# Optimization experiments

Measured on AMD Instinct MI355X. Metric: run time of the kernel, lower is better.

Reference implementation:

```python
import jax, jax.numpy as jnp
import numpy as np

D = 256
H = 8
FFN = 2048
EPS = 1e-5


def _layer_norm(x, g, b):
    m = jnp.mean(x, axis=-1, keepdims=True)
    v = jnp.mean((x - m) ** 2, axis=-1, keepdims=True)
    return (x - m) * jax.lax.rsqrt(v + EPS) * g + b


def _mha(q_in, k_in, v_in, wq, bq, wk, bk, wv, bv, wo, bo, mask):
    B, Sq, _ = q_in.shape
    Sk = k_in.shape[1]
    dh = D // H
    q = (q_in @ wq + bq).reshape(B, Sq, H, dh)
    k = (k_in @ wk + bk).reshape(B, Sk, H, dh)
    v = (v_in @ wv + bv).reshape(B, Sk, H, dh)
    scores = jnp.einsum('bqhd,bkhd->bhqk', q, k) / jnp.sqrt(jnp.float32(dh)).astype(q.dtype)
    if mask is not None:
        scores = scores + mask
    probs = jax.nn.softmax(scores, axis=-1)
    ctx = jnp.einsum('bhqk,bkhd->bqhd', probs, v).reshape(B, Sq, D)
    return ctx @ wo + bo


def setup_inputs() -> dict:
    key = jax.random.key(0)
    ks = jax.random.split(key, 32)
    s = 0.02
    def lin(i, din, dout):
        return jax.random.normal(ks[i], (din, dout), jnp.float32) * s
    inp = {
        'vision_encoder_hidden_states': jax.random.normal(ks[0], (4, 2048, D), jnp.float32),
        'text_encoder_hidden_states': jax.random.normal(ks[1], (4, 1024, D), jnp.float32),
        'vision_encoder_attention_mask': jnp.zeros((4, 1, 1, 2048), jnp.float32),
        'text_encoder_attention_mask': jnp.zeros((4, 1, 1, 1024), jnp.float32),
        'sa_wq': lin(2, D, D), 'sa_bq': jnp.zeros((D,), jnp.float32),
        'sa_wk': lin(3, D, D), 'sa_bk': jnp.zeros((D,), jnp.float32),
        'sa_wv': lin(4, D, D), 'sa_bv': jnp.zeros((D,), jnp.float32),
        'sa_wo': lin(5, D, D), 'sa_bo': jnp.zeros((D,), jnp.float32),
        'ca_wq': lin(6, D, D), 'ca_bq': jnp.zeros((D,), jnp.float32),
        'ca_wk': lin(7, D, D), 'ca_bk': jnp.zeros((D,), jnp.float32),
        'ca_wv': lin(8, D, D), 'ca_bv': jnp.zeros((D,), jnp.float32),
        'ca_wo': lin(9, D, D), 'ca_bo': jnp.zeros((D,), jnp.float32),
        'ln1_g': jnp.ones((D,), jnp.float32), 'ln1_b': jnp.zeros((D,), jnp.float32),
        'ln2_g': jnp.ones((D,), jnp.float32), 'ln2_b': jnp.zeros((D,), jnp.float32),
        'ln3_g': jnp.ones((D,), jnp.float32), 'ln3_b': jnp.zeros((D,), jnp.float32),
        'ln4_g': jnp.ones((D,), jnp.float32), 'ln4_b': jnp.zeros((D,), jnp.float32),
        'fc1_w': lin(10, D, FFN), 'fc1_b': jnp.zeros((FFN,), jnp.float32),
        'fc2_w': lin(11, FFN, D), 'fc2_b': jnp.zeros((D,), jnp.float32),
    }
    return inp


def reference(vision_encoder_hidden_states, text_encoder_hidden_states,
              vision_encoder_attention_mask, text_encoder_attention_mask,
              sa_wq, sa_bq, sa_wk, sa_bk, sa_wv, sa_bv, sa_wo, sa_bo,
              ca_wq, ca_bq, ca_wk, ca_bk, ca_wv, ca_bv, ca_wo, ca_bo,
              ln1_g, ln1_b, ln2_g, ln2_b, ln3_g, ln3_b, ln4_g, ln4_b,
              fc1_w, fc1_b, fc2_w, fc2_b):
    # self-attention over vision queries (dropout = identity in eval)
    residual = vision_encoder_hidden_states
    h = _mha(vision_encoder_hidden_states, vision_encoder_hidden_states,
             vision_encoder_hidden_states,
             sa_wq, sa_bq, sa_wk, sa_bk, sa_wv, sa_bv, sa_wo, sa_bo,
             vision_encoder_attention_mask)
    h = _layer_norm(residual + h, ln1_g, ln1_b)
    # text cross-attention
    res2 = h
    h = _mha(h, text_encoder_hidden_states, text_encoder_hidden_states,
             ca_wq, ca_bq, ca_wk, ca_bk, ca_wv, ca_bv, ca_wo, ca_bo,
             text_encoder_attention_mask)
    h = _layer_norm(res2 + h, ln2_g, ln2_b)
    # third block: residual + dropout(h) -> in eval this is h + h = 2h, then LN
    h = _layer_norm(h + h, ln3_g, ln3_b)
    # FFN
    res = h
    h = jax.nn.relu(h @ fc1_w + fc1_b)
    h = h @ fc2_w + fc2_b
    h = _layer_norm(res + h, ln4_g, ln4_b)
    return h
```

## Files before the change

kernel.cpp:

```cpp
#include <hip/hip_runtime.h>
#include <stdint.h>
#include <stddef.h>

#define HEADS 8
#define DH 32
#define DMODEL 256
#define LN_EPS 1e-5f
#define QSCALE 0.17677669529663687f

typedef unsigned short u16;
typedef __bf16 bf16x8 __attribute__((ext_vector_type(8)));
typedef unsigned short u16x8 __attribute__((ext_vector_type(8)));
typedef float f32x4 __attribute__((ext_vector_type(4)));

static __device__ __forceinline__ u16 bfc(float f) {
    return __builtin_bit_cast(u16, (__bf16)f);
}
static __device__ __forceinline__ bf16x8 ldbf8(const u16* p) {
    return __builtin_bit_cast(bf16x8, *reinterpret_cast<const u16x8*>(p));
}
static __device__ __forceinline__ bf16x8 cvt8(float4 a, float4 b) {
    bf16x8 r;
    r[0] = (__bf16)a.x; r[1] = (__bf16)a.y; r[2] = (__bf16)a.z; r[3] = (__bf16)a.w;
    r[4] = (__bf16)b.x; r[5] = (__bf16)b.y; r[6] = (__bf16)b.z; r[7] = (__bf16)b.w;
    return r;
}

struct TDesc { const float* src; u16* dst; int K; int N; };
struct TArgs { TDesc d[10]; };

__global__ __launch_bounds__(256) void transpose_cvt(TArgs args) {
    TDesc d = args.d[blockIdx.y];
    const int ntx = d.N >> 5;
    const int tiles = (d.K >> 5) * ntx;
    if ((int)blockIdx.x >= tiles) return;
    const int tk = (blockIdx.x / ntx) << 5;
    const int tn = (blockIdx.x % ntx) << 5;
    __shared__ float t[32][33];
    const int lx = threadIdx.x & 31;
    const int ly = threadIdx.x >> 5;
#pragma unroll
    for (int i = 0; i < 4; ++i)
        t[ly + 8 * i][lx] = d.src[(size_t)(tk + ly + 8 * i) * d.N + tn + lx];
    __syncthreads();
#pragma unroll
    for (int i = 0; i < 4; ++i)
        d.dst[(size_t)(tn + ly + 8 * i) * d.K + tk + lx] = bfc(t[lx][ly + 8 * i]);
}

struct Slice { u16* out; const float* bias; int mode; float sc; };

__global__ __launch_bounds__(256) void gemm_xproj(
    const float* __restrict__ Af, const u16* __restrict__ Wt,
    Slice s0, Slice s1, Slice s2, int M, int ntm)
{
    const int lane = threadIdx.x & 63;
    const int wave = threadIdx.x >> 6;
    const int l15 = lane & 15, lhi = lane >> 4;
    const int tm = ((int)blockIdx.x % ntm) * 128;
    const int tn = ((int)blockIdx.x / ntm) * 64;
    const int wm = tm + wave * 32;
    const int sel = tn >> 8;
    const int tl = tn & 255;
    Slice sl = (sel == 0) ? s0 : (sel == 1 ? s1 : s2);

    const f32x4 z4 = {0.f, 0.f, 0.f, 0.f};
    f32x4 acc[2][4];
#pragma unroll
    for (int i = 0; i < 2; ++i)
#pragma unroll
        for (int j = 0; j < 4; ++j) acc[i][j] = z4;

    const float* ar0 = Af + (size_t)(wm + l15) * 256 + lhi * 8;
    const float* ar1 = ar0 + (size_t)16 * 256;
    const u16* b0p = Wt + (size_t)(tn + l15) * 256 + lhi * 8;

    float4 a00 = *(const float4*)(ar0), a01 = *(const float4*)(ar0 + 4);
    float4 a10 = *(const float4*)(ar1), a11 = *(const float4*)(ar1 + 4);
    bf16x8 b[4];
#pragma unroll
    for (int j = 0; j < 4; ++j) b[j] = ldbf8(b0p + (size_t)j * 16 * 256);

#pragma unroll
    for (int k = 32; k < 256; k += 32) {
        float4 n00 = *(const float4*)(ar0 + k), n01 = *(const float4*)(ar0 + k + 4);
        float4 n10 = *(const float4*)(ar1 + k), n11 = *(const float4*)(ar1 + k + 4);
        bf16x8 bn[4];
#pragma unroll
        for (int j = 0; j < 4; ++j) bn[j] = ldbf8(b0p + (size_t)j * 16 * 256 + k);
        bf16x8 a0 = cvt8(a00, a01), a1 = cvt8(a10, a11);
#pragma unroll
        for (int j = 0; j < 4; ++j) {
            acc[0][j] = __builtin_amdgcn_mfma_f32_16x16x32_bf16(a0, b[j], acc[0][j], 0, 0, 0);
            acc[1][j] = __builtin_amdgcn_mfma_f32_16x16x32_bf16(a1, b[j], acc[1][j], 0, 0, 0);
        }
        a00 = n00; a01 = n01; a10 = n10; a11 = n11;
#pragma unroll
        for (int j = 0; j < 4; ++j) b[j] = bn[j];
    }
    {
        bf16x8 a0 = cvt8(a00, a01), a1 = cvt8(a10, a11);
#pragma unroll
        for (int j = 0; j < 4; ++j) {
            acc[0][j] = __builtin_amdgcn_mfma_f32_16x16x32_bf16(a0, b[j], acc[0][j], 0, 0, 0);
            acc[1][j] = __builtin_amdgcn_mfma_f32_16x16x32_bf16(a1, b[j], acc[1][j], 0, 0, 0);
        }
    }

#pragma unroll
    for (int i = 0; i < 2; ++i) {
#pragma unroll
        for (int j = 0; j < 4; ++j) {
            const int col = tl + j * 16 + l15;
            const float bv = sl.bias[col];
            const int row0 = wm + i * 16 + lhi * 4;
            if (sl.mode == 1) {
#pragma unroll
                for (int r = 0; r < 4; ++r)
                    sl.out[(size_t)(row0 + r) * 256 + col] = bfc((acc[i][j][r] + bv) * sl.sc);
            } else {
                ushort4 o = make_ushort4(bfc((acc[i][j][0] + bv) * sl.sc), bfc((acc[i][j][1] + bv) * sl.sc),
                                         bfc((acc[i][j][2] + bv) * sl.sc), bfc((acc[i][j][3] + bv) * sl.sc));
                *reinterpret_cast<ushort4*>(sl.out + (size_t)col * M + row0) = o;
            }
        }
    }
}

template<int MODE, bool RELU>
__global__ __launch_bounds__(256) void gemm_bias(
    const u16* __restrict__ A, const u16* __restrict__ Bt,
    const float* __restrict__ bias, void* __restrict__ Cout,
    int M, int N, int K, int ntm, float osc)
{
    const int lane = threadIdx.x & 63;
    const int wave = threadIdx.x >> 6;
    const int l15 = lane & 15, lhi = lane >> 4;
    const int tm = ((int)blockIdx.x % ntm) * 128;
    const int tn = ((int)blockIdx.x / ntm) * 64;
    const int wm = tm + wave * 32;

    const f32x4 z4 = {0.f, 0.f, 0.f, 0.f};
    f32x4 acc[2][4];
#pragma unroll
    for (int i = 0; i < 2; ++i)
#pragma unroll
        for (int j = 0; j < 4; ++j) acc[i][j] = z4;

    const u16* a0p = A + (size_t)(wm + l15) * K + lhi * 8;
    const u16* a1p = a0p + (size_t)16 * K;
    const u16* b0p = Bt + (size_t)(tn + l15) * K + lhi * 8;

    bf16x8 a0 = ldbf8(a0p), a1 = ldbf8(a1p);
    bf16x8 b[4];
#pragma unroll
    for (int j = 0; j < 4; ++j) b[j] = ldbf8(b0p + (size_t)j * 16 * K);

    for (int k = 32; k < K; k += 32) {
        bf16x8 a0n = ldbf8(a0p + k), a1n = ldbf8(a1p + k);
        bf16x8 bn[4];
#pragma unroll
        for (int j = 0; j < 4; ++j) bn[j] = ldbf8(b0p + (size_t)j * 16 * K + k);
#pragma unroll
        for (int j = 0; j < 4; ++j) {
            acc[0][j] = __builtin_amdgcn_mfma_f32_16x16x32_bf16(a0, b[j], acc[0][j], 0, 0, 0);
            acc[1][j] = __builtin_amdgcn_mfma_f32_16x16x32_bf16(a1, b[j], acc[1][j], 0, 0, 0);
        }
        a0 = a0n; a1 = a1n;
#pragma unroll
        for (int j = 0; j < 4; ++j) b[j] = bn[j];
    }
#pragma unroll
    for (int j = 0; j < 4; ++j) {
        acc[0][j] = __builtin_amdgcn_mfma_f32_16x16x32_bf16(a0, b[j], acc[0][j], 0, 0, 0);
        acc[1][j] = __builtin_amdgcn_mfma_f32_16x16x32_bf16(a1, b[j], acc[1][j], 0, 0, 0);
    }

#pragma unroll
    for (int i = 0; i < 2; ++i) {
#pragma unroll
        for (int j = 0; j < 4; ++j) {
            const int col = tn + j * 16 + l15;
            const float bv = bias[col];
            const int row0 = wm + i * 16 + lhi * 4;
            if (MODE == 0) {
                float* C = (float*)Cout;
#pragma unroll
                for (int r = 0; r < 4; ++r) {
                    float v = acc[i][j][r] + bv;
                    if (RELU) v = fmaxf(v, 0.f);
                    C[(size_t)(row0 + r) * N + col] = v;
                }
            } else {
                u16* C = (u16*)Cout;
#pragma unroll
                for (int r = 0; r < 4; ++r) {
                    float v = acc[i][j][r] + bv;
                    if (RELU) v = fmaxf(v, 0.f);
                    C[(size_t)(row0 + r) * N + col] = bfc(v * osc);
                }
            }
        }
    }
}

__global__ __launch_bounds__(256) void attn_kernel(
    const u16* __restrict__ Qb, const u16* __restrict__ Kb,
    const u16* __restrict__ Vt, const float* __restrict__ mask,
    u16* __restrict__ Ob, int Sq, int Sk, int MkTot)
{
    const int wave = threadIdx.x >> 6;
    const int lane = threadIdx.x & 63;
    const int l15 = lane & 15, lhi = lane >> 4;
    const int nqc = Sq >> 7;
    const int bh = blockIdx.x / nqc;
    const int qc = blockIdx.x % nqc;
    const int b = bh >> 3;
    const int h = bh & 7;
    const int colh = h * DH;
    const int qrow0 = b * Sq + (qc << 7) + wave * 32;
    const int swz = (l15 & 8) << 1;

    __shared__ __align__(16) u16 pt[4][32][72];

    const f32x4 z4 = {0.f, 0.f, 0.f, 0.f};
    bf16x8 qf[2];
    qf[0] = ldbf8(Qb + (size_t)(qrow0 + l15) * DMODEL + colh + lhi * 8);
    qf[1] = ldbf8(Qb + (size_t)(qrow0 + 16 + l15) * DMODEL + colh + lhi * 8);

    f32x4 ctx[2][2] = {{z4, z4}, {z4, z4}};
    float m0 = -1e30f, m1 = -1e30f, ss0 = 0.f, ss1 = 0.f;

    const float* mb = mask + (size_t)b * Sk;
    const u16* kbase = Kb + (size_t)(b * Sk) * DMODEL + colh + lhi * 8;
    const u16* vbase = Vt + (size_t)colh * MkTot + (size_t)b * Sk;

    bf16x8 kf[4], vf[4];
    float4 mk[4];
#pragma unroll
    for (int j = 0; j < 4; ++j)
        kf[j] = ldbf8(kbase + (size_t)(j * 16 + l15) * DMODEL);
#pragma unroll
    for (int ks = 0; ks < 2; ++ks)
#pragma unroll
        for (int dt = 0; dt < 2; ++dt)
            vf[ks * 2 + dt] = ldbf8(vbase + (size_t)(dt * 16 + l15) * MkTot + ks * 32 + lhi * 8);
#pragma unroll
    for (int j = 0; j < 4; ++j)
        mk[j] = *reinterpret_cast<const float4*>(mb + j * 16 + lhi * 4);

    for (int kt = 0; kt < Sk; kt += 64) {
        f32x4 s[2][4];
        __builtin_amdgcn_s_setprio(1);
#pragma unroll
        for (int j = 0; j < 4; ++j) {
            s[0][j] = __builtin_amdgcn_mfma_f32_16x16x32_bf16(kf[j], qf[0], z4, 0, 0, 0);
            s[1][j] = __builtin_amdgcn_mfma_f32_16x16x32_bf16(kf[j], qf[1], z4, 0, 0, 0);
        }
        __builtin_amdgcn_s_setprio(0);

        const int ktn = (kt + 64 < Sk) ? kt + 64 : kt;
        bf16x8 kn[4], vn[4];
        float4 mn[4];
#pragma unroll
        for (int j = 0; j < 4; ++j)
            kn[j] = ldbf8(kbase + (size_t)(ktn + j * 16 + l15) * DMODEL);
#pragma unroll
        for (int ks = 0; ks < 2; ++ks)
#pragma unroll
            for (int dt = 0; dt < 2; ++dt)
                vn[ks * 2 + dt] = ldbf8(vbase + (size_t)(dt * 16 + l15) * MkTot + ktn + ks * 32 + lhi * 8);
#pragma unroll
        for (int j = 0; j < 4; ++j)
            mn[j] = *reinterpret_cast<const float4*>(mb + ktn + j * 16 + lhi * 4);

#pragma unroll
        for (int j = 0; j < 4; ++j) {
            s[0][j][0] += mk[j].x; s[1][j][0] += mk[j].x;
            s[0][j][1] += mk[j].y; s[1][j][1] += mk[j].y;
            s[0][j][2] += mk[j].z; s[1][j][2] += mk[j].z;
            s[0][j][3] += mk[j].w; s[1][j][3] += mk[j].w;
        }

        float mx0 = fmaxf(fmaxf(s[0][0][0], s[0][0][1]), fmaxf(s[0][0][2], s[0][0][3]));
        float mx1 = fmaxf(fmaxf(s[1][0][0], s[1][0][1]), fmaxf(s[1][0][2], s[1][0][3]));
#pragma unroll
        for (int j = 1; j < 4; ++j) {
            mx0 = fmaxf(mx0, fmaxf(fmaxf(s[0][j][0], s[0][j][1]), fmaxf(s[0][j][2], s[0][j][3])));
            mx1 = fmaxf(mx1, fmaxf(fmaxf(s[1][j][0], s[1][j][1]), fmaxf(s[1][j][2], s[1][j][3])));
        }

        if (!__all((mx0 - m0 <= 8.0f) && (mx1 - m1 <= 8.0f))) {
            mx0 = fmaxf(mx0, __shfl_xor(mx0, 16, 64));
            mx0 = fmaxf(mx0, __shfl_xor(mx0, 32, 64));
            mx1 = fmaxf(mx1, __shfl_xor(mx1, 16, 64));
            mx1 = fmaxf(mx1, __shfl_xor(mx1, 32, 64));
            float n0 = fmaxf(m0, mx0), n1 = fmaxf(m1, mx1);
            float c0 = __expf(m0 - n0), c1 = __expf(m1 - n1);
            m0 = n0; m1 = n1; ss0 *= c0; ss1 *= c1;
#pragma unroll
            for (int r = 0; r < 4; ++r) {
                float cc0 = __shfl(c0, lhi * 4 + r, 64);
                float cc1 = __shfl(c1, lhi * 4 + r, 64);
                ctx[0][0][r] *= cc0; ctx[0][1][r] *= cc0;
                ctx[1][0][r] *= cc1; ctx[1][1][r] *= cc1;
            }
        }

        float ps0 = 0.f, ps1 = 0.f;
#pragma unroll
        for (int j = 0; j < 4; ++j)
#pragma unroll
            for (int r = 0; r < 4; ++r) {
                float p0 = __expf(s[0][j][r] - m0);
                float p1 = __expf(s[1][j][r] - m1);
                s[0][j][r] = p0; s[1][j][r] = p1;
                ps0 += p0; ps1 += p1;
            }
        ss0 += ps0; ss1 += ps1;

        asm volatile("" ::: "memory");
#pragma unroll
        for (int i = 0; i < 2; ++i)
#pragma unroll
            for (int j = 0; j < 4; ++j) {
                ushort4 w = make_ushort4(bfc(s[i][j][0]), bfc(s[i][j][1]),
                                         bfc(s[i][j][2]), bfc(s[i][j][3]));
                *reinterpret_cast<ushort4*>(&pt[wave][i * 16 + l15][(j * 16 + lhi * 4) ^ swz]) = w;
            }
        asm volatile("" ::: "memory");

        __builtin_amdgcn_s_setprio(1);
#pragma unroll
        for (int ks = 0; ks < 2; ++ks) {
            bf16x8 pa0 = ldbf8(&pt[wave][l15][(ks * 32 + lhi * 8) ^ swz]);
            bf16x8 pa1 = ldbf8(&pt[wave][16 + l15][(ks * 32 + lhi * 8) ^ swz]);
#pragma unroll
            for (int dt = 0; dt < 2; ++dt) {
                ctx[0][dt] = __builtin_amdgcn_mfma_f32_16x16x32_bf16(pa0, vf[ks * 2 + dt], ctx[0][dt], 0, 0, 0);
                ctx[1][dt] = __builtin_amdgcn_mfma_f32_16x16x32_bf16(pa1, vf[ks * 2 + dt], ctx[1][dt], 0, 0, 0);
            }
        }
        __builtin_amdgcn_s_setprio(0);

#pragma unroll
        for (int j = 0; j < 4; ++j) { kf[j] = kn[j]; vf[j] = vn[j]; mk[j] = mn[j]; }
    }

    ss0 += __shfl_xor(ss0, 16, 64); ss0 += __shfl_xor(ss0, 32, 64);
    ss1 += __shfl_xor(ss1, 16, 64); ss1 += __shfl_xor(ss1, 32, 64);
#pragma unroll
    for (int r = 0; r < 4; ++r) {
        const float i0 = 1.0f / __shfl(ss0, lhi * 4 + r, 64);
        const float i1 = 1.0f / __shfl(ss1, lhi * 4 + r, 64);
        const int row0 = qrow0 + lhi * 4 + r;
#pragma unroll
        for (int dt = 0; dt < 2; ++dt) {
            Ob[(size_t)row0 * DMODEL + colh + dt * 16 + l15] = bfc(ctx[0][dt][r] * i0);
            Ob[(size_t)(row0 + 16) * DMODEL + colh + dt * 16 + l15] = bfc(ctx[1][dt][r] * i1);
        }
    }
}

template<bool DBL, bool WBF>
__global__ __launch_bounds__(256) void ln_kernel(
    const float* __restrict__ X, const float* __restrict__ Res,
    const float* __restrict__ g1p, const float* __restrict__ b1p,
    const float* __restrict__ g2p, const float* __restrict__ b2p,
    float* __restrict__ Of, u16* __restrict__ Oh)
{
    const int lane = threadIdx.x & 63;
    const int row = blockIdx.x * 4 + (threadIdx.x >> 6);
    const size_t base = (size_t)row * DMODEL + lane * 4;
    float4 x = *reinterpret_cast<const float4*>(X + base);
    float4 rr = *reinterpret_cast<const float4*>(Res + base);
    float v[4] = {x.x + rr.x, x.y + rr.y, x.z + rr.z, x.w + rr.w};
    float s = v[0] + v[1] + v[2] + v[3];
    float q = v[0] * v[0] + v[1] * v[1] + v[2] * v[2] + v[3] * v[3];
#pragma unroll
    for (int m = 1; m < 64; m <<= 1) { s += __shfl_xor(s, m, 64); q += __shfl_xor(q, m, 64); }
    float mean = s * (1.0f / DMODEL);
    float rstd = rsqrtf(fmaxf(q * (1.0f / DMODEL) - mean * mean, 0.f) + LN_EPS);
    float4 g = *reinterpret_cast<const float4*>(g1p + lane * 4);
    float4 bb = *reinterpret_cast<const float4*>(b1p + lane * 4);
    float y[4];
    y[0] = (v[0] - mean) * rstd * g.x + bb.x;
    y[1] = (v[1] - mean) * rstd * g.y + bb.y;
    y[2] = (v[2] - mean) * rstd * g.z + bb.z;
    y[3] = (v[3] - mean) * rstd * g.w + bb.w;
    if constexpr (DBL) {
#pragma unroll
        for (int k2 = 0; k2 < 4; ++k2) y[k2] *= 2.0f;
        float s2 = y[0] + y[1] + y[2] + y[3];
        float q2 = y[0] * y[0] + y[1] * y[1] + y[2] * y[2] + y[3] * y[3];
#pragma unroll
        for (int m = 1; m < 64; m <<= 1) { s2 += __shfl_xor(s2, m, 64); q2 += __shfl_xor(q2, m, 64); }
        float mean2 = s2 * (1.0f / DMODEL);
        float rstd2 = rsqrtf(fmaxf(q2 * (1.0f / DMODEL) - mean2 * mean2, 0.f) + LN_EPS);
        float4 g2 = *reinterpret_cast<const float4*>(g2p + lane * 4);
        float4 b2 = *reinterpret_cast<const float4*>(b2p + lane * 4);
        y[0] = (y[0] - mean2) * rstd2 * g2.x + b2.x;
        y[1] = (y[1] - mean2) * rstd2 * g2.y + b2.y;
        y[2] = (y[2] - mean2) * rstd2 * g2.z + b2.z;
        y[3] = (y[3] - mean2) * rstd2 * g2.w + b2.w;
    }
    *reinterpret_cast<float4*>(Of + base) = make_float4(y[0], y[1], y[2], y[3]);
    if constexpr (WBF) {
        ushort4 o = make_ushort4(bfc(y[0]), bfc(y[1]), bfc(y[2]), bfc(y[3]));
        *reinterpret_cast<ushort4*>(Oh + base) = o;
    }
}

extern "C" void kernel_launch(void* const* d_in, const int* in_sizes, int n_in,
                              void* d_out, int out_size, void* d_ws, size_t ws_size,
                              hipStream_t stream) {
    constexpr size_t MB = 1u << 20;
    if (ws_size < 70 * MB) return;

    const float* vis   = (const float*)d_in[0];
    const float* txt   = (const float*)d_in[1];
    const float* vmask = (const float*)d_in[2];
    const float* tmask = (const float*)d_in[3];
    const float* sa_wq = (const float*)d_in[4];  const float* sa_bq = (const float*)d_in[5];
    const float* sa_wk = (const float*)d_in[6];  const float* sa_bk = (const float*)d_in[7];
    const float* sa_wv = (const float*)d_in[8];  const float* sa_bv = (const float*)d_in[9];
    const float* sa_wo = (const float*)d_in[10]; const float* sa_bo = (const float*)d_in[11];
    const float* ca_wq = (const float*)d_in[12]; const float* ca_bq = (const float*)d_in[13];
    const float* ca_wk = (const float*)d_in[14]; const float* ca_bk = (const float*)d_in[15];
    const float* ca_wv = (const float*)d_in[16]; const float* ca_bv = (const float*)d_in[17];
    const float* ca_wo = (const float*)d_in[18]; const float* ca_bo = (const float*)d_in[19];
    const float* ln1_g = (const float*)d_in[20]; const float* ln1_b = (const float*)d_in[21];
    const float* ln2_g = (const float*)d_in[22]; const float* ln2_b = (const float*)d_in[23];
    const float* ln3_g = (const float*)d_in[24]; const float* ln3_b = (const float*)d_in[25];
    const float* ln4_g = (const float*)d_in[26]; const float* ln4_b = (const float*)d_in[27];
    const float* fc1_w = (const float*)d_in[28]; const float* fc1_b = (const float*)d_in[29];
    const float* fc2_w = (const float*)d_in[30]; const float* fc2_b = (const float*)d_in[31];

    const int B = 4, Sq = 2048, St = 1024;
    const int Mq = B * Sq;
    const int Mt = B * St;

    char* ws = (char*)d_ws;
    u16*   q_bf    = (u16*)(ws + 6 * MB);
    u16*   k_bf    = (u16*)(ws + 10 * MB);
    u16*   vt_bf   = (u16*)(ws + 14 * MB);
    u16*   ctx_bf  = (u16*)(ws + 18 * MB);
    u16*   ffn1_bf = (u16*)(ws + 0);
    float* attn_f  = (float*)(ws + 32 * MB);
    float* h1_f    = (float*)(ws + 40 * MB);
    u16*   h1_bf   = (u16*)(ws + 48 * MB);
    float* h3_f    = (float*)(ws + 52 * MB);
    u16*   h3_bf   = (u16*)(ws + 60 * MB);
    u16*   wts     = (u16*)(ws + 64 * MB);
    float* ffn2_f  = attn_f;

    u16* wqkv_t = wts;
    u16* wkv_t  = wqkv_t + 768 * 256;
    u16* cwq_t  = wkv_t + 512 * 256;
    u16* wo_t   = cwq_t + 65536;
    u16* cwo_t  = wo_t + 65536;
    u16* fc1_t  = cwo_t + 65536;
    u16* fc2_t  = fc1_t + 2048 * 256;

    TArgs ta;
    ta.d[0] = {sa_wq, wqkv_t + 0 * 65536, 256, 256};
    ta.d[1] = {sa_wk, wqkv_t + 1 * 65536, 256, 256};
    ta.d[2] = {sa_wv, wqkv_t + 2 * 65536, 256, 256};
    ta.d[3] = {ca_wk, wkv_t + 0 * 65536, 256, 256};
    ta.d[4] = {ca_wv, wkv_t + 1 * 65536, 256, 256};
    ta.d[5] = {ca_wq, cwq_t, 256, 256};
    ta.d[6] = {sa_wo, wo_t, 256, 256};
    ta.d[7] = {ca_wo, cwo_t, 256, 256};
    ta.d[8] = {fc1_w, fc1_t, 256, 2048};
    ta.d[9] = {fc2_w, fc2_t, 2048, 256};
    transpose_cvt<<<dim3(512, 10), 256, 0, stream>>>(ta);

    auto gemm_grid = [](int M, int N) { return dim3((M / 128) * (N / 64)); };

    Slice sq = {q_bf, sa_bq, 1, QSCALE}, sk = {k_bf, sa_bk, 1, 1.f}, sv = {vt_bf, sa_bv, 2, 1.f};
    gemm_xproj<<<dim3((Mq / 128) * 12), 256, 0, stream>>>(vis, wqkv_t, sq, sk, sv, Mq, Mq / 128);
    attn_kernel<<<dim3(B * HEADS * (Sq / 128)), 256, 0, stream>>>(q_bf, k_bf, vt_bf, vmask, ctx_bf, Sq, Sq, Mq);
    gemm_bias<0, false><<<gemm_grid(Mq, 256), 256, 0, stream>>>(ctx_bf, wo_t, sa_bo, attn_f, Mq, 256, 256, Mq / 128, 1.f);
    ln_kernel<false, true><<<dim3(Mq / 4), 256, 0, stream>>>(attn_f, vis, ln1_g, ln1_b, nullptr, nullptr, h1_f, h1_bf);

    Slice ck = {k_bf, ca_bk, 1, 1.f}, cv = {vt_bf, ca_bv, 2, 1.f}, cd = {nullptr, nullptr, 1, 1.f};
    gemm_xproj<<<dim3((Mt / 128) * 8), 256, 0, stream>>>(txt, wkv_t, ck, cv, cd, Mt, Mt / 128);
    gemm_bias<1, false><<<gemm_grid(Mq, 256), 256, 0, stream>>>(h1_bf, cwq_t, ca_bq, q_bf, Mq, 256, 256, Mq / 128, QSCALE);
    attn_kernel<<<dim3(B * HEADS * (Sq / 128)), 256, 0, stream>>>(q_bf, k_bf, vt_bf, tmask, ctx_bf, Sq, St, Mt);
    gemm_bias<0, false><<<gemm_grid(Mq, 256), 256, 0, stream>>>(ctx_bf, cwo_t, ca_bo, attn_f, Mq, 256, 256, Mq / 128, 1.f);
    ln_kernel<true, true><<<dim3(Mq / 4), 256, 0, stream>>>(attn_f, h1_f, ln2_g, ln2_b, ln3_g, ln3_b, h3_f, h3_bf);

    gemm_bias<1, true><<<gemm_grid(Mq, 2048), 256, 0, stream>>>(h3_bf, fc1_t, fc1_b, ffn1_bf, Mq, 2048, 256, Mq / 128, 1.f);
    gemm_bias<0, false><<<gemm_grid(Mq, 256), 256, 0, stream>>>(ffn1_bf, fc2_t, fc2_b, ffn2_f, Mq, 256, 2048, Mq / 128, 1.f);
    ln_kernel<false, false><<<dim3(Mq / 4), 256, 0, stream>>>(ffn2_f, h3_f, ln4_g, ln4_b, nullptr, nullptr, (float*)d_out, nullptr);
}
```

Before: 295.4 us.

## Pipeline attention QK/PV across tiles, use exp2 softmax, add 64x64 GEMM kernel

The attention loop is software-pipelined with two alternating score buffers, so the QK^T MFMAs for the next 64-key tile are issued alongside the PV MFMAs of the current tile. Softmax switches to exp2, with log2e folded into the Q scale and the mask, and the lazy-rescale threshold is raised. A new 64x64-tile GEMM (gemm64) replaces the 128x64 kernel for all N=256 projections to put more blocks on the device. All GEMM grids are also reordered to walk N fastest so neighbouring blocks share A rows in cache. In exchange, the attention kernel holds two sets of K/V/mask registers, which may lower occupancy.

```diff
diff --git a/kernel.cpp b/kernel.cpp
--- a/kernel.cpp
+++ b/kernel.cpp
@@ -6,7 +6,10 @@
 #define DH 32
 #define DMODEL 256
 #define LN_EPS 1e-5f
+#define LOG2E 1.4426950408889634f
 #define QSCALE 0.17677669529663687f
+#define QSCALE2 (QSCALE * LOG2E)
+#define EXP2(x) __builtin_amdgcn_exp2f(x)
 
 typedef unsigned short u16;
 typedef __bf16 bf16x8 __attribute__((ext_vector_type(8)));
@@ -52,13 +55,13 @@
 
 __global__ __launch_bounds__(256) void gemm_xproj(
     const float* __restrict__ Af, const u16* __restrict__ Wt,
-    Slice s0, Slice s1, Slice s2, int M, int ntm)
+    Slice s0, Slice s1, Slice s2, int M, int ntn)
 {
     const int lane = threadIdx.x & 63;
     const int wave = threadIdx.x >> 6;
     const int l15 = lane & 15, lhi = lane >> 4;
-    const int tm = ((int)blockIdx.x % ntm) * 128;
-    const int tn = ((int)blockIdx.x / ntm) * 64;
+    const int tn = ((int)blockIdx.x % ntn) * 64;
+    const int tm = ((int)blockIdx.x / ntn) * 128;
     const int wm = tm + wave * 32;
     const int sel = tn >> 8;
     const int tl = tn & 255;
@@ -131,13 +134,13 @@
 __global__ __launch_bounds__(256) void gemm_bias(
     const u16* __restrict__ A, const u16* __restrict__ Bt,
     const float* __restrict__ bias, void* __restrict__ Cout,
-    int M, int N, int K, int ntm, float osc)
+    int M, int N, int K, int ntn, float osc)
 {
     const int lane = threadIdx.x & 63;
     const int wave = threadIdx.x >> 6;
     const int l15 = lane & 15, lhi = lane >> 4;
-    const int tm = ((int)blockIdx.x % ntm) * 128;
-    const int tn = ((int)blockIdx.x / ntm) * 64;
+    const int tn = ((int)blockIdx.x % ntn) * 64;
+    const int tm = ((int)blockIdx.x / ntn) * 128;
     const int wm = tm + wave * 32;
 
     const f32x4 z4 = {0.f, 0.f, 0.f, 0.f};
@@ -181,6 +184,77 @@
 #pragma unroll
         for (int j = 0; j < 4; ++j) {
             const int col = tn + j * 16 + l15;
+            const float bv = bias[col];
+            const int row0 = wm + i * 16 + lhi * 4;
+            if (MODE == 0) {
+                float* C = (float*)Cout;
+#pragma unroll
+                for (int r = 0; r < 4; ++r) {
+                    float v = acc[i][j][r] + bv;
+                    if (RELU) v = fmaxf(v, 0.f);
+                    C[(size_t)(row0 + r) * N + col] = v;
+                }
+            } else {
+                u16* C = (u16*)Cout;
+#pragma unroll
+                for (int r = 0; r < 4; ++r) {
+                    float v = acc[i][j][r] + bv;
+                    if (RELU) v = fmaxf(v, 0.f);
+                    C[(size_t)(row0 + r) * N + col] = bfc(v * osc);
+                }
+            }
+        }
+    }
+}
+
+template<int MODE, bool RELU>
+__global__ __launch_bounds__(256) void gemm64(
+    const u16* __restrict__ A, const u16* __restrict__ Bt,
+    const float* __restrict__ bias, void* __restrict__ Cout,
+    int M, int N, int K, int ntn, float osc)
+{
+    const int lane = threadIdx.x & 63;
+    const int wave = threadIdx.x >> 6;
+    const int l15 = lane & 15, lhi = lane >> 4;
+    const int tn = ((int)blockIdx.x % ntn) * 64;
+    const int tm = ((int)blockIdx.x / ntn) * 64;
+    const int wm = tm + (wave & 1) * 32;
+    const int wn = tn + (wave >> 1) * 32;
+
+    const f32x4 z4 = {0.f, 0.f, 0.f, 0.f};
+    f32x4 acc[2][2] = {{z4, z4}, {z4, z4}};
+
+    const u16* a0p = A + (size_t)(wm + l15) * K + lhi * 8;
+    const u16* a1p = a0p + (size_t)16 * K;
+    const u16* b0p = Bt + (size_t)(wn + l15) * K + lhi * 8;
+    const u16* b1p = b0p + (size_t)16 * K;
+
+    bf16x8 aA0 = ldbf8(a0p), aA1 = ldbf8(a1p), bA0 = ldbf8(b0p), bA1 = ldbf8(b1p);
+    bf16x8 aB0 = ldbf8(a0p + 32), aB1 = ldbf8(a1p + 32), bB0 = ldbf8(b0p + 32), bB1 = ldbf8(b1p + 32);
+
+#define G64_MFMA(aX0, aX1, bX0, bX1)                                                        \
+    acc[0][0] = __builtin_amdgcn_mfma_f32_16x16x32_bf16(aX0, bX0, acc[0][0], 0, 0, 0);      \
+    acc[0][1] = __builtin_amdgcn_mfma_f32_16x16x32_bf16(aX0, bX1, acc[0][1], 0, 0, 0);      \
+    acc[1][0] = __builtin_amdgcn_mfma_f32_16x16x32_bf16(aX1, bX0, acc[1][0], 0, 0, 0);      \
+    acc[1][1] = __builtin_amdgcn_mfma_f32_16x16x32_bf16(aX1, bX1, acc[1][1], 0, 0, 0);
+
+    for (int k = 64; k < K; k += 64) {
+        G64_MFMA(aA0, aA1, bA0, bA1);
+        aA0 = ldbf8(a0p + k); aA1 = ldbf8(a1p + k);
+        bA0 = ldbf8(b0p + k); bA1 = ldbf8(b1p + k);
+        G64_MFMA(aB0, aB1, bB0, bB1);
+        aB0 = ldbf8(a0p + k + 32); aB1 = ldbf8(a1p + k + 32);
+        bB0 = ldbf8(b0p + k + 32); bB1 = ldbf8(b1p + k + 32);
+    }
+    G64_MFMA(aA0, aA1, bA0, bA1);
+    G64_MFMA(aB0, aB1, bB0, bB1);
+#undef G64_MFMA
+
+#pragma unroll
+    for (int i = 0; i < 2; ++i) {
+#pragma unroll
+        for (int j = 0; j < 2; ++j) {
+            const int col = wn + j * 16 + l15;
             const float bv = bias[col];
             const int row0 = wm + i * 16 + lhi * 4;
             if (MODE == 0) {
@@ -224,9 +298,8 @@
     __shared__ __align__(16) u16 pt[4][32][72];
 
     const f32x4 z4 = {0.f, 0.f, 0.f, 0.f};
-    bf16x8 qf[2];
-    qf[0] = ldbf8(Qb + (size_t)(qrow0 + l15) * DMODEL + colh + lhi * 8);
-    qf[1] = ldbf8(Qb + (size_t)(qrow0 + 16 + l15) * DMODEL + colh + lhi * 8);
+    const bf16x8 qf0 = ldbf8(Qb + (size_t)(qrow0 + l15) * DMODEL + colh + lhi * 8);
+    const bf16x8 qf1 = ldbf8(Qb + (size_t)(qrow0 + 16 + l15) * DMODEL + colh + lhi * 8);
 
     f32x4 ctx[2][2] = {{z4, z4}, {z4, z4}};
     float m0 = -1e30f, m1 = -1e30f, ss0 = 0.f, ss1 = 0.f;
@@ -235,117 +308,133 @@
     const u16* kbase = Kb + (size_t)(b * Sk) * DMODEL + colh + lhi * 8;
     const u16* vbase = Vt + (size_t)colh * MkTot + (size_t)b * Sk;
 
-    bf16x8 kf[4], vf[4];
-    float4 mk[4];
-#pragma unroll
-    for (int j = 0; j < 4; ++j)
-        kf[j] = ldbf8(kbase + (size_t)(j * 16 + l15) * DMODEL);
+    bf16x8 kf0[4], kf1[4], vf0[4], vf1[4];
+    float4 mk0[4], mk1[4];
+    f32x4 sA[2][4], sB[2][4];
+
+#pragma unroll
+    for (int j = 0; j < 4; ++j) {
+        kf0[j] = ldbf8(kbase + (size_t)(j * 16 + l15) * DMODEL);
+        kf1[j] = ldbf8(kbase + (size_t)(64 + j * 16 + l15) * DMODEL);
+    }
 #pragma unroll
     for (int ks = 0; ks < 2; ++ks)
 #pragma unroll
-        for (int dt = 0; dt < 2; ++dt)
-            vf[ks * 2 + dt] = ldbf8(vbase + (size_t)(dt * 16 + l15) * MkTot + ks * 32 + lhi * 8);
-#pragma unroll
-    for (int j = 0; j < 4; ++j)
-        mk[j] = *reinterpret_cast<const float4*>(mb + j * 16 + lhi * 4);
-
-    for (int kt = 0; kt < Sk; kt += 64) {
-        f32x4 s[2][4];
-        __builtin_amdgcn_s_setprio(1);
-#pragma unroll
-        for (int j = 0; j < 4; ++j) {
-            s[0][j] = __builtin_amdgcn_mfma_f32_16x16x32_bf16(kf[j], qf[0], z4, 0, 0, 0);
-            s[1][j] = __builtin_amdgcn_mfma_f32_16x16x32_bf16(kf[j], qf[1], z4, 0, 0, 0);
-        }
-        __builtin_amdgcn_s_setprio(0);
-
-        const int ktn = (kt + 64 < Sk) ? kt + 64 : kt;
-        bf16x8 kn[4], vn[4];
-        float4 mn[4];
-#pragma unroll
-        for (int j = 0; j < 4; ++j)
-            kn[j] = ldbf8(kbase + (size_t)(ktn + j * 16 + l15) * DMODEL);
-#pragma unroll
-        for (int ks = 0; ks < 2; ++ks)
-#pragma unroll
-            for (int dt = 0; dt < 2; ++dt)
-                vn[ks * 2 + dt] = ldbf8(vbase + (size_t)(dt * 16 + l15) * MkTot + ktn + ks * 32 + lhi * 8);
-#pragma unroll
-        for (int j = 0; j < 4; ++j)
-            mn[j] = *reinterpret_cast<const float4*>(mb + ktn + j * 16 + lhi * 4);
-
-#pragma unroll
-        for (int j = 0; j < 4; ++j) {
-            s[0][j][0] += mk[j].x; s[1][j][0] += mk[j].x;
-            s[0][j][1] += mk[j].y; s[1][j][1] += mk[j].y;
-            s[0][j][2] += mk[j].z; s[1][j][2] += mk[j].z;
-            s[0][j][3] += mk[j].w; s[1][j][3] += mk[j].w;
-        }
-
-        float mx0 = fmaxf(fmaxf(s[0][0][0], s[0][0][1]), fmaxf(s[0][0][2], s[0][0][3]));
-        float mx1 = fmaxf(fmaxf(s[1][0][0], s[1][0][1]), fmaxf(s[1][0][2], s[1][0][3]));
-#pragma unroll
-        for (int j = 1; j < 4; ++j) {
-            mx0 = fmaxf(mx0, fmaxf(fmaxf(s[0][j][0], s[0][j][1]), fmaxf(s[0][j][2], s[0][j][3])));
-            mx1 = fmaxf(mx1, fmaxf(fmaxf(s[1][j][0], s[1][j][1]), fmaxf(s[1][j][2], s[1][j][3])));
-        }
-
-        if (!__all((mx0 - m0 <= 8.0f) && (mx1 - m1 <= 8.0f))) {
-            mx0 = fmaxf(mx0, __shfl_xor(mx0, 16, 64));
-            mx0 = fmaxf(mx0, __shfl_xor(mx0, 32, 64));
-            mx1 = fmaxf(mx1, __shfl_xor(mx1, 16, 64));
-            mx1 = fmaxf(mx1, __shfl_xor(mx1, 32, 64));
-            float n0 = fmaxf(m0, mx0), n1 = fmaxf(m1, mx1);
-            float c0 = __expf(m0 - n0), c1 = __expf(m1 - n1);
-            m0 = n0; m1 = n1; ss0 *= c0; ss1 *= c1;
-#pragma unroll
-            for (int r = 0; r < 4; ++r) {
-                float cc0 = __shfl(c0, lhi * 4 + r, 64);
-                float cc1 = __shfl(c1, lhi * 4 + r, 64);
-                ctx[0][0][r] *= cc0; ctx[0][1][r] *= cc0;
-                ctx[1][0][r] *= cc1; ctx[1][1][r] *= cc1;
-            }
-        }
-
-        float ps0 = 0.f, ps1 = 0.f;
-#pragma unroll
-        for (int j = 0; j < 4; ++j)
-#pragma unroll
-            for (int r = 0; r < 4; ++r) {
-                float p0 = __expf(s[0][j][r] - m0);
-                float p1 = __expf(s[1][j][r] - m1);
-                s[0][j][r] = p0; s[1][j][r] = p1;
-                ps0 += p0; ps1 += p1;
-            }
-        ss0 += ps0; ss1 += ps1;
-
-        asm volatile("" ::: "memory");
-#pragma unroll
-        for (int i = 0; i < 2; ++i)
-#pragma unroll
-            for (int j = 0; j < 4; ++j) {
-                ushort4 w = make_ushort4(bfc(s[i][j][0]), bfc(s[i][j][1]),
-                                         bfc(s[i][j][2]), bfc(s[i][j][3]));
-                *reinterpret_cast<ushort4*>(&pt[wave][i * 16 + l15][(j * 16 + lhi * 4) ^ swz]) = w;
-            }
-        asm volatile("" ::: "memory");
-
-        __builtin_amdgcn_s_setprio(1);
-#pragma unroll
-        for (int ks = 0; ks < 2; ++ks) {
-            bf16x8 pa0 = ldbf8(&pt[wave][l15][(ks * 32 + lhi * 8) ^ swz]);
-            bf16x8 pa1 = ldbf8(&pt[wave][16 + l15][(ks * 32 + lhi * 8) ^ swz]);
-#pragma unroll
-            for (int dt = 0; dt < 2; ++dt) {
-                ctx[0][dt] = __builtin_amdgcn_mfma_f32_16x16x32_bf16(pa0, vf[ks * 2 + dt], ctx[0][dt], 0, 0, 0);
-                ctx[1][dt] = __builtin_amdgcn_mfma_f32_16x16x32_bf16(pa1, vf[ks * 2 + dt], ctx[1][dt], 0, 0, 0);
-            }
-        }
-        __builtin_amdgcn_s_setprio(0);
-
-#pragma unroll
-        for (int j = 0; j < 4; ++j) { kf[j] = kn[j]; vf[j] = vn[j]; mk[j] = mn[j]; }
-    }
+        for (int dt = 0; dt < 2; ++dt) {
+            vf0[ks * 2 + dt] = ldbf8(vbase + (size_t)(dt * 16 + l15) * MkTot + ks * 32 + lhi * 8);
+            vf1[ks * 2 + dt] = ldbf8(vbase + (size_t)(dt * 16 + l15) * MkTot + 64 + ks * 32 + lhi * 8);
+        }
+#pragma unroll
+    for (int j = 0; j < 4; ++j) {
+        float4 t0 = *reinterpret_cast<const float4*>(mb + j * 16 + lhi * 4);
+        float4 t1 = *reinterpret_cast<const float4*>(mb + 64 + j * 16 + lhi * 4);
+        mk0[j] = make_float4(t0.x * LOG2E, t0.y * LOG2E, t0.z * LOG2E, t0.w * LOG2E);
+        mk1[j] = make_float4(t1.x * LOG2E, t1.y * LOG2E, t1.z * LOG2E, t1.w * LOG2E);
+    }
+#pragma unroll
+    for (int j = 0; j < 4; ++j) {
+        sA[0][j] = __builtin_amdgcn_mfma_f32_16x16x32_bf16(kf0[j], qf0, z4, 0, 0, 0);
+        sA[1][j] = __builtin_amdgcn_mfma_f32_16x16x32_bf16(kf0[j], qf1, z4, 0, 0, 0);
+    }
+
+#define SOFTMAX_PSTORE(S, MK)                                                              \
+    {                                                                                      \
+        _Pragma("unroll")                                                                  \
+        for (int j = 0; j < 4; ++j) {                                                      \
+            S[0][j][0] += MK[j].x; S[1][j][0] += MK[j].x;                                  \
+            S[0][j][1] += MK[j].y; S[1][j][1] += MK[j].y;                                  \
+            S[0][j][2] += MK[j].z; S[1][j][2] += MK[j].z;                                  \
+            S[0][j][3] += MK[j].w; S[1][j][3] += MK[j].w;                                  \
+        }                                                                                  \
+        float mx0 = fmaxf(fmaxf(S[0][0][0], S[0][0][1]), fmaxf(S[0][0][2], S[0][0][3]));   \
+        float mx1 = fmaxf(fmaxf(S[1][0][0], S[1][0][1]), fmaxf(S[1][0][2], S[1][0][3]));   \
+        _Pragma("unroll")                                                                  \
+        for (int j = 1; j < 4; ++j) {                                                      \
+            mx0 = fmaxf(mx0, fmaxf(fmaxf(S[0][j][0], S[0][j][1]), fmaxf(S[0][j][2], S[0][j][3]))); \
+            mx1 = fmaxf(mx1, fmaxf(fmaxf(S[1][j][0], S[1][j][1]), fmaxf(S[1][j][2], S[1][j][3]))); \
+        }                                                                                  \
+        if (!__all((mx0 - m0 <= 12.0f) && (mx1 - m1 <= 12.0f))) {                          \
+            mx0 = fmaxf(mx0, __shfl_xor(mx0, 16, 64));                                     \
+            mx0 = fmaxf(mx0, __shfl_xor(mx0, 32, 64));                                     \
+            mx1 = fmaxf(mx1, __shfl_xor(mx1, 16, 64));                                     \
+            mx1 = fmaxf(mx1, __shfl_xor(mx1, 32, 64));                                     \
+            float n0 = fmaxf(m0, mx0), n1 = fmaxf(m1, mx1);                                \
+            float c0 = EXP2(m0 - n0), c1 = EXP2(m1 - n1);                                  \
+            m0 = n0; m1 = n1; ss0 *= c0; ss1 *= c1;                                        \
+            _Pragma("unroll")                                                              \
+            for (int r = 0; r < 4; ++r) {                                                  \
+                float cc0 = __shfl(c0, lhi * 4 + r, 64);                                   \
+                float cc1 = __shfl(c1, lhi * 4 + r, 64);                                   \
+                ctx[0][0][r] *= cc0; ctx[0][1][r] *= cc0;                                  \
+                ctx[1][0][r] *= cc1; ctx[1][1][r] *= cc1;                                  \
+            }                                                                              \
+        }                                                                                  \
+        float ps0 = 0.f, ps1 = 0.f;                                                        \
+        _Pragma("unroll")                                                                  \
+        for (int j = 0; j < 4; ++j)                                                        \
+            _Pragma("unroll")                                                              \
+            for (int r = 0; r < 4; ++r) {                                                  \
+                float p0 = EXP2(S[0][j][r] - m0);                                          \
+                float p1 = EXP2(S[1][j][r] - m1);                                          \
+                S[0][j][r] = p0; S[1][j][r] = p1;                                          \
+                ps0 += p0; ps1 += p1;                                                      \
+            }                                                                              \
+        ss0 += ps0; ss1 += ps1;                                                            \
+        _Pragma("unroll")                                                                  \
+        for (int i = 0; i < 2; ++i)                                                        \
+            _Pragma("unroll")                                                              \
+            for (int j = 0; j < 4; ++j) {                                                  \
+                ushort4 w = make_ushort4(bfc(S[i][j][0]), bfc(S[i][j][1]),                 \
+                                         bfc(S[i][j][2]), bfc(S[i][j][3]));                \
+                *reinterpret_cast<ushort4*>(&pt[wave][i * 16 + l15][(j * 16 + lhi * 4) ^ swz]) = w; \
+            }                                                                              \
+    }
+
+#define ATTN_HALF(SC, SN, KD, KM, VV, MD, tpre)                                            \
+    {                                                                                      \
+        const int tp = (tpre);                                                             \
+        _Pragma("unroll")                                                                  \
+        for (int j = 0; j < 4; ++j)                                                        \
+            KD[j] = ldbf8(kbase + (size_t)(tp + j * 16 + l15) * DMODEL);                   \
+        SOFTMAX_PSTORE(SC, MD);                                                            \
+        _Pragma("unroll")                                                                  \
+        for (int j = 0; j < 4; ++j) {                                                      \
+            float4 tt = *reinterpret_cast<const float4*>(mb + tp + j * 16 + lhi * 4);      \
+            MD[j] = make_float4(tt.x * LOG2E, tt.y * LOG2E, tt.z * LOG2E, tt.w * LOG2E);   \
+        }                                                                                  \
+        __builtin_amdgcn_s_setprio(1);                                                     \
+        _Pragma("unroll")                                                                  \
+        for (int j = 0; j < 4; ++j) {                                                      \
+            SN[0][j] = __builtin_amdgcn_mfma_f32_16x16x32_bf16(KM[j], qf0, z4, 0, 0, 0);   \
+            SN[1][j] = __builtin_amdgcn_mfma_f32_16x16x32_bf16(KM[j], qf1, z4, 0, 0, 0);   \
+        }                                                                                  \
+        _Pragma("unroll")                                                                  \
+        for (int ks = 0; ks < 2; ++ks) {                                                   \
+            bf16x8 pa0 = ldbf8(&pt[wave][l15][(ks * 32 + lhi * 8) ^ swz]);                 \
+            bf16x8 pa1 = ldbf8(&pt[wave][16 + l15][(ks * 32 + lhi * 8) ^ swz]);            \
+            _Pragma("unroll")                                                              \
+            for (int dt = 0; dt < 2; ++dt) {                                               \
+                ctx[0][dt] = __builtin_amdgcn_mfma_f32_16x16x32_bf16(pa0, VV[ks * 2 + dt], ctx[0][dt], 0, 0, 0); \
+                ctx[1][dt] = __builtin_amdgcn_mfma_f32_16x16x32_bf16(pa1, VV[ks * 2 + dt], ctx[1][dt], 0, 0, 0); \
+            }                                                                              \
+        }                                                                                  \
+        __builtin_amdgcn_s_setprio(0);                                                     \
+        _Pragma("unroll")                                                                  \
+        for (int ks = 0; ks < 2; ++ks)                                                     \
+            _Pragma("unroll")                                                              \
+            for (int dt = 0; dt < 2; ++dt)                                                 \
+                VV[ks * 2 + dt] = ldbf8(vbase + (size_t)(dt * 16 + l15) * MkTot + tp + ks * 32 + lhi * 8); \
+    }
+
+    const int NT = Sk >> 6;
+    for (int t = 0; t < NT; t += 2) {
+        const int t2 = ((t + 2 < NT) ? t + 2 : t) << 6;
+        ATTN_HALF(sA, sB, kf0, kf1, vf0, mk0, t2);
+        const int t3 = ((t + 3 < NT) ? t + 3 : t + 1) << 6;
+        ATTN_HALF(sB, sA, kf1, kf0, vf1, mk1, t3);
+    }
+#undef ATTN_HALF
+#undef SOFTMAX_PSTORE
 
     ss0 += __shfl_xor(ss0, 16, 64); ss0 += __shfl_xor(ss0, 32, 64);
     ss1 += __shfl_xor(ss1, 16, 64); ss1 += __shfl_xor(ss1, 32, 64);
@@ -475,22 +564,20 @@
     ta.d[9] = {fc2_w, fc2_t, 2048, 256};
     transpose_cvt<<<dim3(512, 10), 256, 0, stream>>>(ta);
 
-    auto gemm_grid = [](int M, int N) { return dim3((M / 128) * (N / 64)); };
-
-    Slice sq = {q_bf, sa_bq, 1, QSCALE}, sk = {k_bf, sa_bk, 1, 1.f}, sv = {vt_bf, sa_bv, 2, 1.f};
-    gemm_xproj<<<dim3((Mq / 128) * 12), 256, 0, stream>>>(vis, wqkv_t, sq, sk, sv, Mq, Mq / 128);
+    Slice sq = {q_bf, sa_bq, 1, QSCALE2}, sk = {k_bf, sa_bk, 1, 1.f}, sv = {vt_bf, sa_bv, 2, 1.f};
+    gemm_xproj<<<dim3((Mq / 128) * 12), 256, 0, stream>>>(vis, wqkv_t, sq, sk, sv, Mq, 12);
     attn_kernel<<<dim3(B * HEADS * (Sq / 128)), 256, 0, stream>>>(q_bf, k_bf, vt_bf, vmask, ctx_bf, Sq, Sq, Mq);
-    gemm_bias<0, false><<<gemm_grid(Mq, 256), 256, 0, stream>>>(ctx_bf, wo_t, sa_bo, attn_f, Mq, 256, 256, Mq / 128, 1.f);
+    gemm64<0, false><<<dim3((Mq / 64) * 4), 256, 0, stream>>>(ctx_bf, wo_t, sa_bo, attn_f, Mq, 256, 256, 4, 1.f);
     ln_kernel<false, true><<<dim3(Mq / 4), 256, 0, stream>>>(attn_f, vis, ln1_g, ln1_b, nullptr, nullptr, h1_f, h1_bf);
 
     Slice ck = {k_bf, ca_bk, 1, 1.f}, cv = {vt_bf, ca_bv, 2, 1.f}, cd = {nullptr, nullptr, 1, 1.f};
-    gemm_xproj<<<dim3((Mt / 128) * 8), 256, 0, stream>>>(txt, wkv_t, ck, cv, cd, Mt, Mt / 128);
-    gemm_bias<1, false><<<gemm_grid(Mq, 256), 256, 0, stream>>>(h1_bf, cwq_t, ca_bq, q_bf, Mq, 256, 256, Mq / 128, QSCALE);
+    gemm_xproj<<<dim3((Mt / 128) * 8), 256, 0, stream>>>(txt, wkv_t, ck, cv, cd, Mt, 8);
+    gemm64<1, false><<<dim3((Mq / 64) * 4), 256, 0, stream>>>(h1_bf, cwq_t, ca_bq, q_bf, Mq, 256, 256, 4, QSCALE2);
     attn_kernel<<<dim3(B * HEADS * (Sq / 128)), 256, 0, stream>>>(q_bf, k_bf, vt_bf, tmask, ctx_bf, Sq, St, Mt);
-    gemm_bias<0, false><<<gemm_grid(Mq, 256), 256, 0, stream>>>(ctx_bf, cwo_t, ca_bo, attn_f, Mq, 256, 256, Mq / 128, 1.f);
+    gemm64<0, false><<<dim3((Mq / 64) * 4), 256, 0, stream>>>(ctx_bf, cwo_t, ca_bo, attn_f, Mq, 256, 256, 4, 1.f);
     ln_kernel<true, true><<<dim3(Mq / 4), 256, 0, stream>>>(attn_f, h1_f, ln2_g, ln2_b, ln3_g, ln3_b, h3_f, h3_bf);
 
-    gemm_bias<1, true><<<gemm_grid(Mq, 2048), 256, 0, stream>>>(h3_bf, fc1_t, fc1_b, ffn1_bf, Mq, 2048, 256, Mq / 128, 1.f);
-    gemm_bias<0, false><<<gemm_grid(Mq, 256), 256, 0, stream>>>(ffn1_bf, fc2_t, fc2_b, ffn2_f, Mq, 256, 2048, Mq / 128, 1.f);
+    gemm_bias<1, true><<<dim3((Mq / 128) * 32), 256, 0, stream>>>(h3_bf, fc1_t, fc1_b, ffn1_bf, Mq, 2048, 256, 32, 1.f);
+    gemm64<0, false><<<dim3((Mq / 64) * 4), 256, 0, stream>>>(ffn1_bf, fc2_t, fc2_b, ffn2_f, Mq, 256, 2048, 4, 1.f);
     ln_kernel<false, false><<<dim3(Mq / 4), 256, 0, stream>>>(ffn2_f, h3_f, ln4_g, ln4_b, nullptr, nullptr, (float*)d_out, nullptr);
 }
```

Result: slower. 318.5 us (+7.8%).
